# Kernel optimization log

Hardware: AMD Instinct MI355X
Metric: run time of the kernel (lower is better)

The kernel has to match this reference:

```python
import jax, jax.numpy as jnp
import numpy as np

B, N, D = 4, 512, 256  # batch, num_diseases, feature_dim == hidden_dim
H = 256                # hidden_dim
EPS = 1e-5

def _layernorm(x, g, b):
    m = jnp.mean(x, axis=-1, keepdims=True)
    v = jnp.mean((x - m) ** 2, axis=-1, keepdims=True)
    return (x - m) * jax.lax.rsqrt(v + EPS) * g + b

def setup_inputs() -> dict:
    key = jax.random.key(0)
    ks = jax.random.split(key, 16)
    s = 0.02
    return {
        "x": jax.random.normal(ks[0], (B, N, D), jnp.float32),
        "area_matrix": jax.random.uniform(ks[1], (B, N), jnp.float32),
        "co_occurrence": jax.random.uniform(ks[2], (N, N), jnp.float32),
        "Wq": jax.random.normal(ks[3], (H, D), jnp.float32) * s,
        "bq": jnp.zeros((H,), jnp.float32),
        "Wk": jax.random.normal(ks[4], (H, D), jnp.float32) * s,
        "bk": jnp.zeros((H,), jnp.float32),
        "Wv": jax.random.normal(ks[5], (H, D), jnp.float32) * s,
        "bv": jnp.zeros((H,), jnp.float32),
        "We1": jax.random.normal(ks[6], (H, 2), jnp.float32) * 0.5,
        "be1": jnp.zeros((H,), jnp.float32),
        "We2": jax.random.normal(ks[7], (1, H), jnp.float32) * s,
        "be2": jnp.zeros((1,), jnp.float32),
        "Wo": jax.random.normal(ks[8], (H, H), jnp.float32) * s,
        "bo": jnp.zeros((H,), jnp.float32),
        "g_ot": jnp.ones((H,), jnp.float32),
        "b_ot": jnp.zeros((H,), jnp.float32),
        "g1": jnp.ones((H,), jnp.float32),
        "b1": jnp.zeros((H,), jnp.float32),
        "g2": jnp.ones((H,), jnp.float32),
        "b2": jnp.zeros((H,), jnp.float32),
    }

def reference(x, area_matrix, co_occurrence, Wq, bq, Wk, bk, Wv, bv,
              We1, be1, We2, be2, Wo, bo, g_ot, b_ot, g1, b1, g2, b2):
    # projections: (B, N, H)
    q = jnp.einsum('bnd,hd->bnh', x, Wq) + bq
    k = jnp.einsum('bnd,hd->bnh', x, Wk) + bk
    v = jnp.einsum('bnd,hd->bnh', x, Wv) + bv
    attn_scores = jnp.einsum('bih,bjh->bij', q, k) / jnp.sqrt(jnp.float32(H))
    # edge inputs: (B, N, N, 2) = stack(broadcast area along last N, broadcast co-occ along batch)
    area = jnp.broadcast_to(area_matrix[:, :, None], (B, N, N))
    co = jnp.broadcast_to(co_occurrence[None], (B, N, N))
    edge_inputs = jnp.stack([area, co], axis=-1)
    h = jax.nn.relu(jnp.einsum('bije,he->bijh', edge_inputs, We1) + be1)
    edge_weights = jax.nn.sigmoid(jnp.einsum('bijh,oh->bijo', h, We2) + be2)[..., 0]
    attn_probs = jax.nn.softmax(attn_scores * edge_weights, axis=-1)  # dropout = identity (eval)
    out = jnp.einsum('bij,bjh->bih', attn_probs, v)
    out = _layernorm(out, g1, b1)
    out = jax.nn.relu(_layernorm(jnp.einsum('bnh,oh->bno', out, Wo) + bo, g_ot, b_ot))
    out = _layernorm(out + x, g2, b2)
    return out
```

## Files before the change

kernel.cpp:

```cpp
#include <hip/hip_runtime.h>

typedef unsigned short u16;
typedef unsigned int u32;

#define NB 4
#define NN 512
#define ND 256
#define NH 256
#define TI 4

typedef __attribute__((ext_vector_type(8))) short short8;
typedef __attribute__((ext_vector_type(4))) float f32x4;

typedef __attribute__((address_space(3))) u32 lds32_t;
typedef __attribute__((address_space(1))) const u32 g32_t;
__device__ __forceinline__ void pf16(const void* gp, u32* lp) {
    __builtin_amdgcn_global_load_lds((g32_t*)gp, (lds32_t*)lp, 16, 0, 0);
}

__device__ __forceinline__ u16 bfq(float f) {
    u32 t; __builtin_memcpy(&t, &f, 4);
    u32 r = (t + 0x7FFFu + ((t >> 16) & 1u)) >> 16;
    return (u16)r;
}

__device__ __forceinline__ float waveReduceSum(float v) {
#pragma unroll
    for (int o = 32; o > 0; o >>= 1) v += __shfl_down(v, o);
    return v;
}

__device__ __forceinline__ void blockReduce8(float4& va, float4& vb, float4* red) {
#pragma unroll
    for (int o = 32; o > 0; o >>= 1) {
        va.x += __shfl_down(va.x, o); va.y += __shfl_down(va.y, o);
        va.z += __shfl_down(va.z, o); va.w += __shfl_down(va.w, o);
        vb.x += __shfl_down(vb.x, o); vb.y += __shfl_down(vb.y, o);
        vb.z += __shfl_down(vb.z, o); vb.w += __shfl_down(vb.w, o);
    }
    int wid = threadIdx.x >> 6;
    __syncthreads();
    if ((threadIdx.x & 63) == 0) { red[2 * wid] = va; red[2 * wid + 1] = vb; }
    __syncthreads();
    float4 ra = red[0], rb = red[1];
#pragma unroll
    for (int w = 1; w < 8; ++w) {
        float4 ua = red[2 * w], ub = red[2 * w + 1];
        ra.x += ua.x; ra.y += ua.y; ra.z += ua.z; ra.w += ua.w;
        rb.x += ub.x; rb.y += ub.y; rb.z += ub.z; rb.w += ub.w;
    }
    va = ra; vb = rb;
}

__global__ __launch_bounds__(256) void prep_kernel(
    const float* __restrict__ x, const float* __restrict__ Wq,
    const float* __restrict__ Wk, const float* __restrict__ Wv,
    const float* __restrict__ Wo,
    u16* __restrict__ xb, u16* __restrict__ wb)
{
    const int idx4 = (blockIdx.x * 256 + threadIdx.x) * 4;
    const float* src;
    u16* dst;
    int off;
    if (idx4 < 524288) { src = x; dst = xb; off = idx4; }
    else {
        int u = idx4 - 524288;
        int which = u >> 16; off = u & 65535;
        src = (which == 0) ? Wq : (which == 1) ? Wk : (which == 2) ? Wv : Wo;
        dst = wb + which * 65536;
    }
    float4 f = *(const float4*)(src + off);
    u32 lo = (u32)bfq(f.x) | ((u32)bfq(f.y) << 16);
    u32 hi = (u32)bfq(f.z) | ((u32)bfq(f.w) << 16);
    *(uint2*)(dst + off) = make_uint2(lo, hi);
}

__global__ __launch_bounds__(256) void qkv_mfma(
    const u16* __restrict__ xb, const u16* __restrict__ wb,
    const float* __restrict__ bq, const float* __restrict__ bk, const float* __restrict__ bv,
    u16* __restrict__ qb, u16* __restrict__ kb, u16* __restrict__ vt)
{
    const int lane = threadIdx.x & 63, wave = threadIdx.x >> 6;
    const int r0 = blockIdx.x * 64 + wave * 16;
    const int out0 = blockIdx.y * 16;
    const int which = blockIdx.y >> 4;
    const float* bia = (which == 0) ? bq : (which == 1) ? bk : bv;

    __shared__ u32 pfdummy[256];

    {
        const u16* apre = xb + (size_t)(blockIdx.x * 64 + wave * 16) * 256;
#pragma unroll
        for (int q = 0; q < 8; ++q) pf16(apre + q * 512 + lane * 8, pfdummy);
        const u16* bpre = wb + which * 65536 + (size_t)((out0 & 255) + wave * 4) * 256;
#pragma unroll
        for (int q = 0; q < 2; ++q) pf16(bpre + q * 512 + lane * 8, pfdummy);
    }

    const int m = lane & 15, koff = (lane >> 4) * 8;
    const u16* Ap = xb + (size_t)(r0 + m) * 256 + koff;
    const u16* Bp = wb + which * 65536 + (size_t)((out0 & 255) + m) * 256 + koff;

    f32x4 acc = {0.f, 0.f, 0.f, 0.f};
#pragma unroll
    for (int ks = 0; ks < 8; ++ks) {
        short8 a  = *(const short8*)(Ap + ks * 32);
        short8 bb = *(const short8*)(Bp + ks * 32);
        acc = __builtin_amdgcn_mfma_f32_16x16x32_bf16(a, bb, acc, 0, 0, 0);
    }

    const int oc = (out0 + m) & 255;
    const float bias = bia[oc];
    const int rbase = r0 + (lane >> 4) * 4;
#pragma unroll
    for (int reg = 0; reg < 4; ++reg) {
        int R = rbase + reg;
        u16 val = bfq(acc[reg] + bias);
        if (which == 0)      qb[(size_t)R * 256 + oc] = val;
        else if (which == 1) kb[(size_t)R * 256 + oc] = val;
        else                 vt[((size_t)(R >> 9) * 256 + oc) * 512 + (R & 511)] = val;
    }
}

#define PSTR 520
#define YSTR 264
__global__ __launch_bounds__(512, 4) void fused_kernel(
    const float* __restrict__ x, const float* __restrict__ area, const float* __restrict__ co,
    const float* __restrict__ We1, const float* __restrict__ be1,
    const float* __restrict__ We2, const float* __restrict__ be2,
    const u16* __restrict__ wob, const float* __restrict__ bo,
    const float* __restrict__ g_ot, const float* __restrict__ b_ot,
    const float* __restrict__ g1, const float* __restrict__ b1,
    const float* __restrict__ g2, const float* __restrict__ b2,
    const u16* __restrict__ qb, const u16* __restrict__ kb,
    const u16* __restrict__ vt, float* __restrict__ out)
{
    const int tid = threadIdx.x;
    const int bsw = (blockIdx.x & 7) * 64 + (blockIdx.x >> 3);
    const int b = bsw >> 7;
    const int i0 = (bsw & 127) << 2;
    const int lane = tid & 63, w = tid >> 6;
    const int g = lane >> 4, c = lane & 15;
    const int hP = tid & 255, half = tid >> 8;

    __shared__ float histS[1024], histB[1024];
    __shared__ float pvbuf[1024];
    __shared__ u16 srow16[16 * PSTR];
    __shared__ u16 y16[16 * YSTR];
    __shared__ float4 red8b[16];
    __shared__ float sBaseS[4], sBaseB[4], redA[8], redB[8];
    __shared__ u32 pfdummy[256];

    const int m = lane & 15, koff = (lane >> 4) * 8;
    const u16* Ap    = qb + (size_t)(b * 512 + i0 + m) * 256 + koff;
    const u16* Kbase = kb + (size_t)(b * 512 + m) * 256 + koff;

    short8 afr[8];
#pragma unroll
    for (int ks = 0; ks < 8; ++ks) afr[ks] = *(const short8*)(Ap + ks * 32);

    float cov[4];
#pragma unroll
    for (int t = 0; t < 4; ++t)
        cov[t] = co[(size_t)(i0 + g) * NN + (w * 4 + t) * 16 + c];

    float xv[TI];
#pragma unroll
    for (int ti = 0; ti < TI; ++ti)
        xv[ti] = x[(size_t)(b * NN + i0 + ti) * ND + hP];

    const float bov  = bo[hP];
    const float g1v  = g1[hP],  b1v  = b1[hP];
    const float gotv = g_ot[hP], botv = b_ot[hP];
    const float g2v  = g2[hP],  b2v  = b2[hP];
    const float be2f = be2[0];

    {
        const u16* kpre = kb + (size_t)(b * 512 + w * 64) * 256;
#pragma unroll
        for (int q = 0; q < 32; ++q) pf16(kpre + q * 512 + lane * 8, pfdummy);
        const u16* vpre = vt + (size_t)(b * 256 + w * 32) * 512;
#pragma unroll
        for (int q = 0; q < 32; ++q) pf16(vpre + q * 512 + lane * 8, pfdummy);
        const u16* wpre = wob + (size_t)(w * 32) * 256;
#pragma unroll
        for (int q = 0; q < 16; ++q) pf16(wpre + q * 512 + lane * 8, pfdummy);
        pf16(co + (size_t)(i0 + (w >> 1)) * 512 + (w & 1) * 256 + lane * 4, pfdummy);
    }

    histS[tid] = 0.f; histS[tid + 512] = 0.f;
    histB[tid] = 0.f; histB[tid + 512] = 0.f;
    {
        u32* s32 = (u32*)srow16;
        for (int i = tid; i < 4160; i += 512) s32[i] = 0u;
        u32* y32 = (u32*)y16;
        for (int i = tid; i < 2112; i += 512) y32[i] = 0u;
    }
    __syncthreads();

    {
        const int s = tid >> 7, h0 = tid & 127;
        const float a = area[b * NN + i0 + s];
        float baS = 0.f, baB = 0.f;
#pragma unroll
        for (int k = 0; k < 2; ++k) {
            const int h = h0 + 128 * k;
            const float w10 = We1[2 * h], w11 = We1[2 * h + 1];
            const float w2v = We2[h], be1v = be1[h];
            const float al = fmaf(a, w10, be1v);
            const float sl = w11 * w2v, bb = al * w2v;
            if (w11 == 0.f) {
                if (al > 0.f) baB += bb;
            } else {
                float tt = -al / w11;
                if (w11 > 0.f) {
                    if (tt <= 0.f)      { baS += sl; baB += bb; }
                    else if (tt < 1.f) {
                        int u = (int)(tt * 256.f); u = u > 255 ? 255 : u;
                        atomicAdd(&histS[s * 256 + u], sl);
                        atomicAdd(&histB[s * 256 + u], bb);
                    }
                } else {
                    if (tt >= 1.f)      { baS += sl; baB += bb; }
                    else if (tt > 0.f) {
                        baS += sl; baB += bb;
                        int u = (int)(tt * 256.f); u = u > 255 ? 255 : u;
                        atomicAdd(&histS[s * 256 + u], -sl);
                        atomicAdd(&histB[s * 256 + u], -bb);
                    }
                }
            }
        }
        float rS = waveReduceSum(baS), rB = waveReduceSum(baB);
        if (lane == 0) { redA[w] = rS; redB[w] = rB; }
    }

    f32x4 sacc[4];
    {
#pragma unroll
        for (int t = 0; t < 4; ++t) {
            const u16* Bp = Kbase + (size_t)(w * 4 + t) * 16 * 256;
            f32x4 acc = {0.f, 0.f, 0.f, 0.f};
#pragma unroll
            for (int ks = 0; ks < 8; ++ks) {
                short8 bb = *(const short8*)(Bp + ks * 32);
                acc = __builtin_amdgcn_mfma_f32_16x16x32_bf16(afr[ks], bb, acc, 0, 0, 0);
            }
            sacc[t] = acc;
        }
    }
    __syncthreads();
    if (tid < 4) {
        sBaseS[tid] = redA[2 * tid] + redA[2 * tid + 1];
        sBaseB[tid] = redB[2 * tid] + redB[2 * tid + 1];
    }

    {
        const int s = w & 3;
        float* hp = (w < 4) ? histS : histB;
        float b0 = hp[s * 256 + 4 * lane + 0];
        float b1 = hp[s * 256 + 4 * lane + 1];
        float b2 = hp[s * 256 + 4 * lane + 2];
        float b3 = hp[s * 256 + 4 * lane + 3];
        float p0 = b0, p1 = p0 + b1, p2 = p1 + b2, p3 = p2 + b3;
        float incl = p3;
#pragma unroll
        for (int off = 1; off < 64; off <<= 1) {
            float t = __shfl_up(incl, off);
            if (lane >= off) incl += t;
        }
        float excl = incl - p3;
        hp[s * 256 + 4 * lane + 0] = p0 + excl;
        hp[s * 256 + 4 * lane + 1] = p1 + excl;
        hp[s * 256 + 4 * lane + 2] = p2 + excl;
        hp[s * 256 + 4 * lane + 3] = p3 + excl;
    }
    __syncthreads();

    {
#pragma unroll
        for (int t = 0; t < 4; ++t) {
            const int j = (w * 4 + t) * 16 + c;
            float s0 = __shfl(sacc[t][0], c);
            float s1 = __shfl(sacc[t][1], c);
            float s2 = __shfl(sacc[t][2], c);
            float s3 = __shfl(sacc[t][3], c);
            float sv = (g == 0) ? s0 : (g == 1) ? s1 : (g == 2) ? s2 : s3;
            float cc = cov[t];
            int u = (int)(cc * 256.f); u = u > 255 ? 255 : u;
            float Sg = sBaseS[g] + histS[g * 256 + u];
            float Bg = sBaseB[g] + histB[g * 256 + u];
            float e = fmaf(cc, Sg, Bg) + be2f;
            float ew = 1.f / (1.f + __expf(-e));
            srow16[g * PSTR + j] = bfq(__expf(sv * 0.0625f * ew));
        }
    }
    __syncthreads();

    {
        const int t0 = 2 * w, t1 = 2 * w + 1;
        const u16* B0p = vt + ((size_t)(b * 256 + t0 * 16 + m)) * 512 + koff;
        const u16* B1p = vt + ((size_t)(b * 256 + t1 * 16 + m)) * 512 + koff;
        const u16* Arow = srow16 + m * PSTR + koff;
        f32x4 acc0 = {0.f, 0.f, 0.f, 0.f}, acc1 = {0.f, 0.f, 0.f, 0.f};
#pragma unroll
        for (int ks = 0; ks < 16; ++ks) {
            short8 a  = *(const short8*)(Arow + ks * 32);
            short8 b0 = *(const short8*)(B0p + ks * 32);
            short8 b1 = *(const short8*)(B1p + ks * 32);
            acc0 = __builtin_amdgcn_mfma_f32_16x16x32_bf16(a, b0, acc0, 0, 0, 0);
            acc1 = __builtin_amdgcn_mfma_f32_16x16x32_bf16(a, b1, acc1, 0, 0, 0);
        }
        if (lane < 16) {
#pragma unroll
            for (int reg = 0; reg < 4; ++reg) {
                pvbuf[reg * 256 + t0 * 16 + lane] = acc0[reg];
                pvbuf[reg * 256 + t1 * 16 + lane] = acc1[reg];
            }
        }
        __syncthreads();
    }

    float4 sa, sb;
    float accv[TI];
#pragma unroll
    for (int ti = 0; ti < TI; ++ti) {
        accv[ti] = (half == 0) ? pvbuf[ti * 256 + hP] : 0.f;
        ((float*)&sa)[ti] = accv[ti];
        ((float*)&sb)[ti] = accv[ti] * accv[ti];
    }
    blockReduce8(sa, sb, red8b);
    if (half == 0) {
#pragma unroll
        for (int ti = 0; ti < TI; ++ti) {
            float mean = ((const float*)&sa)[ti] * (1.f / 256.f);
            float var = fmaxf(((const float*)&sb)[ti] * (1.f / 256.f) - mean * mean, 0.f);
            y16[ti * YSTR + hP] = bfq((accv[ti] - mean) * rsqrtf(var + 1e-5f) * g1v + b1v);
        }
    }
    __syncthreads();

    {
        const int t0 = 2 * w, t1 = 2 * w + 1;
        const u16* B0p = wob + (size_t)(t0 * 16 + m) * 256 + koff;
        const u16* B1p = wob + (size_t)(t1 * 16 + m) * 256 + koff;
        const u16* Arow = y16 + m * YSTR + koff;
        f32x4 acc0 = {0.f, 0.f, 0.f, 0.f}, acc1 = {0.f, 0.f, 0.f, 0.f};
#pragma unroll
        for (int ks = 0; ks < 8; ++ks) {
            short8 a  = *(const short8*)(Arow + ks * 32);
            short8 b0 = *(const short8*)(B0p + ks * 32);
            short8 b1 = *(const short8*)(B1p + ks * 32);
            acc0 = __builtin_amdgcn_mfma_f32_16x16x32_bf16(a, b0, acc0, 0, 0, 0);
            acc1 = __builtin_amdgcn_mfma_f32_16x16x32_bf16(a, b1, acc1, 0, 0, 0);
        }
        if (lane < 16) {
#pragma unroll
            for (int reg = 0; reg < 4; ++reg) {
                pvbuf[reg * 256 + t0 * 16 + lane] = acc0[reg];
                pvbuf[reg * 256 + t1 * 16 + lane] = acc1[reg];
            }
        }
        __syncthreads();
    }

    float acc2[TI];
#pragma unroll
    for (int ti = 0; ti < TI; ++ti) {
        acc2[ti] = (half == 0) ? pvbuf[ti * 256 + hP] + bov : 0.f;
        ((float*)&sa)[ti] = acc2[ti];
        ((float*)&sb)[ti] = acc2[ti] * acc2[ti];
    }
    blockReduce8(sa, sb, red8b);
    float z[TI];
#pragma unroll
    for (int ti = 0; ti < TI; ++ti) {
        float mean = ((const float*)&sa)[ti] * (1.f / 256.f);
        float var = fmaxf(((const float*)&sb)[ti] * (1.f / 256.f) - mean * mean, 0.f);
        z[ti] = fmaxf((acc2[ti] - mean) * rsqrtf(var + 1e-5f) * gotv + botv, 0.f);
    }

    float tt[TI];
#pragma unroll
    for (int ti = 0; ti < TI; ++ti) {
        tt[ti] = (half == 0) ? z[ti] + xv[ti] : 0.f;
        ((float*)&sa)[ti] = tt[ti]; ((float*)&sb)[ti] = tt[ti] * tt[ti];
    }
    blockReduce8(sa, sb, red8b);
    if (half == 0) {
#pragma unroll
        for (int ti = 0; ti < TI; ++ti) {
            float mean = ((const float*)&sa)[ti] * (1.f / 256.f);
            float var = fmaxf(((const float*)&sb)[ti] * (1.f / 256.f) - mean * mean, 0.f);
            float o = (tt[ti] - mean) * rsqrtf(var + 1e-5f) * g2v + b2v;
            out[(size_t)(b * NN + i0 + ti) * NH + hP] = o;
        }
    }
}

extern "C" void kernel_launch(void* const* d_in, const int* in_sizes, int n_in,
                              void* d_out, int out_size, void* d_ws, size_t ws_size,
                              hipStream_t stream) {
    const float* x    = (const float*)d_in[0];
    const float* area = (const float*)d_in[1];
    const float* co   = (const float*)d_in[2];
    const float* Wq   = (const float*)d_in[3];
    const float* bq   = (const float*)d_in[4];
    const float* Wk   = (const float*)d_in[5];
    const float* bk   = (const float*)d_in[6];
    const float* Wv   = (const float*)d_in[7];
    const float* bv   = (const float*)d_in[8];
    const float* We1  = (const float*)d_in[9];
    const float* be1  = (const float*)d_in[10];
    const float* We2  = (const float*)d_in[11];
    const float* be2  = (const float*)d_in[12];
    const float* Wo   = (const float*)d_in[13];
    const float* bo   = (const float*)d_in[14];
    const float* g_ot = (const float*)d_in[15];
    const float* b_ot = (const float*)d_in[16];
    const float* g1   = (const float*)d_in[17];
    const float* b1   = (const float*)d_in[18];
    const float* g2   = (const float*)d_in[19];
    const float* b2   = (const float*)d_in[20];

    u16*  xb  = (u16*)d_ws;
    u16*  wb  = xb + (size_t)2048 * 256;
    u16*  qb  = wb + (size_t)4 * 65536;
    u16*  kb  = qb + (size_t)2048 * 256;
    u16*  vt  = kb + (size_t)2048 * 256;

    prep_kernel<<<768, 256, 0, stream>>>(x, Wq, Wk, Wv, Wo, xb, wb);
    qkv_mfma<<<dim3(32, 48), 256, 0, stream>>>(xb, wb, bq, bk, bv, qb, kb, vt);
    fused_kernel<<<NB * NN / TI, 512, 0, stream>>>(x, area, co, We1, be1, We2, be2,
                                                   wb + 3 * 65536, bo,
                                                   g_ot, b_ot, g1, b1, g2, b2,
                                                   qb, kb, vt, (float*)d_out);
}
```

Measured before the change: 172.5 us.

## Merge prep, QKV projection and attention into one kernel with grid barriers

The three launches (bf16 conversion, QKV MFMA projection, fused attention) become one persistent kernel of 512 blocks. Two software grid barriers built on atomics separate the phases, and the edge-MLP histogram work now runs before the first barrier wait so it overlaps the conversion. The aim is to remove launch gaps and inter-kernel drain, at the cost of a memset per call, spin-wait barriers that assume all 512 blocks are co-resident, and dropping the LDS prefetch hints.

```diff
diff --git a/kernel.cpp b/kernel.cpp
--- a/kernel.cpp
+++ b/kernel.cpp
@@ -8,15 +8,10 @@
 #define ND 256
 #define NH 256
 #define TI 4
+#define NBLK 512
 
 typedef __attribute__((ext_vector_type(8))) short short8;
 typedef __attribute__((ext_vector_type(4))) float f32x4;
-
-typedef __attribute__((address_space(3))) u32 lds32_t;
-typedef __attribute__((address_space(1))) const u32 g32_t;
-__device__ __forceinline__ void pf16(const void* gp, u32* lp) {
-    __builtin_amdgcn_global_load_lds((g32_t*)gp, (lds32_t*)lp, 16, 0, 0);
-}
 
 __device__ __forceinline__ u16 bfq(float f) {
     u32 t; __builtin_memcpy(&t, &f, 4);
@@ -52,96 +47,46 @@
     va = ra; vb = rb;
 }
 
-__global__ __launch_bounds__(256) void prep_kernel(
-    const float* __restrict__ x, const float* __restrict__ Wq,
-    const float* __restrict__ Wk, const float* __restrict__ Wv,
-    const float* __restrict__ Wo,
-    u16* __restrict__ xb, u16* __restrict__ wb)
-{
-    const int idx4 = (blockIdx.x * 256 + threadIdx.x) * 4;
-    const float* src;
-    u16* dst;
-    int off;
-    if (idx4 < 524288) { src = x; dst = xb; off = idx4; }
-    else {
-        int u = idx4 - 524288;
-        int which = u >> 16; off = u & 65535;
-        src = (which == 0) ? Wq : (which == 1) ? Wk : (which == 2) ? Wv : Wo;
-        dst = wb + which * 65536;
-    }
-    float4 f = *(const float4*)(src + off);
-    u32 lo = (u32)bfq(f.x) | ((u32)bfq(f.y) << 16);
-    u32 hi = (u32)bfq(f.z) | ((u32)bfq(f.w) << 16);
-    *(uint2*)(dst + off) = make_uint2(lo, hi);
-}
-
-__global__ __launch_bounds__(256) void qkv_mfma(
-    const u16* __restrict__ xb, const u16* __restrict__ wb,
-    const float* __restrict__ bq, const float* __restrict__ bk, const float* __restrict__ bv,
-    u16* __restrict__ qb, u16* __restrict__ kb, u16* __restrict__ vt)
-{
-    const int lane = threadIdx.x & 63, wave = threadIdx.x >> 6;
-    const int r0 = blockIdx.x * 64 + wave * 16;
-    const int out0 = blockIdx.y * 16;
-    const int which = blockIdx.y >> 4;
-    const float* bia = (which == 0) ? bq : (which == 1) ? bk : bv;
-
-    __shared__ u32 pfdummy[256];
-
-    {
-        const u16* apre = xb + (size_t)(blockIdx.x * 64 + wave * 16) * 256;
-#pragma unroll
-        for (int q = 0; q < 8; ++q) pf16(apre + q * 512 + lane * 8, pfdummy);
-        const u16* bpre = wb + which * 65536 + (size_t)((out0 & 255) + wave * 4) * 256;
-#pragma unroll
-        for (int q = 0; q < 2; ++q) pf16(bpre + q * 512 + lane * 8, pfdummy);
-    }
-
-    const int m = lane & 15, koff = (lane >> 4) * 8;
-    const u16* Ap = xb + (size_t)(r0 + m) * 256 + koff;
-    const u16* Bp = wb + which * 65536 + (size_t)((out0 & 255) + m) * 256 + koff;
-
-    f32x4 acc = {0.f, 0.f, 0.f, 0.f};
-#pragma unroll
-    for (int ks = 0; ks < 8; ++ks) {
-        short8 a  = *(const short8*)(Ap + ks * 32);
-        short8 bb = *(const short8*)(Bp + ks * 32);
-        acc = __builtin_amdgcn_mfma_f32_16x16x32_bf16(a, bb, acc, 0, 0, 0);
-    }
-
-    const int oc = (out0 + m) & 255;
-    const float bias = bia[oc];
-    const int rbase = r0 + (lane >> 4) * 4;
-#pragma unroll
-    for (int reg = 0; reg < 4; ++reg) {
-        int R = rbase + reg;
-        u16 val = bfq(acc[reg] + bias);
-        if (which == 0)      qb[(size_t)R * 256 + oc] = val;
-        else if (which == 1) kb[(size_t)R * 256 + oc] = val;
-        else                 vt[((size_t)(R >> 9) * 256 + oc) * 512 + (R & 511)] = val;
-    }
+__device__ __forceinline__ void gbar_arrive(u32* c) {
+    __syncthreads();
+    if (threadIdx.x == 0)
+        __hip_atomic_fetch_add(c, 1u, __ATOMIC_RELEASE, __HIP_MEMORY_SCOPE_AGENT);
+}
+__device__ __forceinline__ void gbar_wait(u32* c, u32 n) {
+    if (threadIdx.x == 0) {
+        while (__hip_atomic_load(c, __ATOMIC_ACQUIRE, __HIP_MEMORY_SCOPE_AGENT) < n)
+            __builtin_amdgcn_s_sleep(2);
+    }
+    __syncthreads();
+    __threadfence();
 }
 
 #define PSTR 520
 #define YSTR 264
-__global__ __launch_bounds__(512, 4) void fused_kernel(
+__global__ __launch_bounds__(512, 4) void mono_kernel(
     const float* __restrict__ x, const float* __restrict__ area, const float* __restrict__ co,
+    const float* __restrict__ Wq, const float* __restrict__ bq,
+    const float* __restrict__ Wk, const float* __restrict__ bk,
+    const float* __restrict__ Wv, const float* __restrict__ bv,
     const float* __restrict__ We1, const float* __restrict__ be1,
     const float* __restrict__ We2, const float* __restrict__ be2,
-    const u16* __restrict__ wob, const float* __restrict__ bo,
+    const float* __restrict__ Wo, const float* __restrict__ bo,
     const float* __restrict__ g_ot, const float* __restrict__ b_ot,
     const float* __restrict__ g1, const float* __restrict__ b1,
     const float* __restrict__ g2, const float* __restrict__ b2,
-    const u16* __restrict__ qb, const u16* __restrict__ kb,
-    const u16* __restrict__ vt, float* __restrict__ out)
+    u16* __restrict__ xb, u16* __restrict__ wb,
+    u16* __restrict__ qb, u16* __restrict__ kb, u16* __restrict__ vt,
+    u32* __restrict__ bar, float* __restrict__ out)
 {
     const int tid = threadIdx.x;
+    const int lane = tid & 63, w = tid >> 6;
+    const int m = lane & 15, koff = (lane >> 4) * 8;
+    const int g = lane >> 4, c = lane & 15;
+    const int hP = tid & 255, half = tid >> 8;
+
     const int bsw = (blockIdx.x & 7) * 64 + (blockIdx.x >> 3);
     const int b = bsw >> 7;
     const int i0 = (bsw & 127) << 2;
-    const int lane = tid & 63, w = tid >> 6;
-    const int g = lane >> 4, c = lane & 15;
-    const int hP = tid & 255, half = tid >> 8;
 
     __shared__ float histS[1024], histB[1024];
     __shared__ float pvbuf[1024];
@@ -149,26 +94,15 @@
     __shared__ u16 y16[16 * YSTR];
     __shared__ float4 red8b[16];
     __shared__ float sBaseS[4], sBaseB[4], redA[8], redB[8];
-    __shared__ u32 pfdummy[256];
-
-    const int m = lane & 15, koff = (lane >> 4) * 8;
-    const u16* Ap    = qb + (size_t)(b * 512 + i0 + m) * 256 + koff;
-    const u16* Kbase = kb + (size_t)(b * 512 + m) * 256 + koff;
-
-    short8 afr[8];
-#pragma unroll
-    for (int ks = 0; ks < 8; ++ks) afr[ks] = *(const short8*)(Ap + ks * 32);
 
     float cov[4];
 #pragma unroll
     for (int t = 0; t < 4; ++t)
         cov[t] = co[(size_t)(i0 + g) * NN + (w * 4 + t) * 16 + c];
-
     float xv[TI];
 #pragma unroll
     for (int ti = 0; ti < TI; ++ti)
         xv[ti] = x[(size_t)(b * NN + i0 + ti) * ND + hP];
-
     const float bov  = bo[hP];
     const float g1v  = g1[hP],  b1v  = b1[hP];
     const float gotv = g_ot[hP], botv = b_ot[hP];
@@ -176,17 +110,24 @@
     const float be2f = be2[0];
 
     {
-        const u16* kpre = kb + (size_t)(b * 512 + w * 64) * 256;
-#pragma unroll
-        for (int q = 0; q < 32; ++q) pf16(kpre + q * 512 + lane * 8, pfdummy);
-        const u16* vpre = vt + (size_t)(b * 256 + w * 32) * 512;
-#pragma unroll
-        for (int q = 0; q < 32; ++q) pf16(vpre + q * 512 + lane * 8, pfdummy);
-        const u16* wpre = wob + (size_t)(w * 32) * 256;
-#pragma unroll
-        for (int q = 0; q < 16; ++q) pf16(wpre + q * 512 + lane * 8, pfdummy);
-        pf16(co + (size_t)(i0 + (w >> 1)) * 512 + (w & 1) * 256 + lane * 4, pfdummy);
-    }
+        const int gtid = blockIdx.x * 512 + tid;
+        const int idx4 = gtid * 4;
+        if (idx4 < 786432) {
+            const float* src; u16* dst; int off;
+            if (idx4 < 524288) { src = x; dst = xb; off = idx4; }
+            else {
+                int u = idx4 - 524288;
+                int which = u >> 16; off = u & 65535;
+                src = (which == 0) ? Wq : (which == 1) ? Wk : (which == 2) ? Wv : Wo;
+                dst = wb + which * 65536;
+            }
+            float4 f = *(const float4*)(src + off);
+            u32 lo = (u32)bfq(f.x) | ((u32)bfq(f.y) << 16);
+            u32 hi = (u32)bfq(f.z) | ((u32)bfq(f.w) << 16);
+            *(uint2*)(dst + off) = make_uint2(lo, hi);
+        }
+    }
+    gbar_arrive(bar);
 
     histS[tid] = 0.f; histS[tid + 512] = 0.f;
     histB[tid] = 0.f; histB[tid + 512] = 0.f;
@@ -197,7 +138,6 @@
         for (int i = tid; i < 2112; i += 512) y32[i] = 0u;
     }
     __syncthreads();
-
     {
         const int s = tid >> 7, h0 = tid & 127;
         const float a = area[b * NN + i0 + s];
@@ -234,27 +174,11 @@
         float rS = waveReduceSum(baS), rB = waveReduceSum(baB);
         if (lane == 0) { redA[w] = rS; redB[w] = rB; }
     }
-
-    f32x4 sacc[4];
-    {
-#pragma unroll
-        for (int t = 0; t < 4; ++t) {
-            const u16* Bp = Kbase + (size_t)(w * 4 + t) * 16 * 256;
-            f32x4 acc = {0.f, 0.f, 0.f, 0.f};
-#pragma unroll
-            for (int ks = 0; ks < 8; ++ks) {
-                short8 bb = *(const short8*)(Bp + ks * 32);
-                acc = __builtin_amdgcn_mfma_f32_16x16x32_bf16(afr[ks], bb, acc, 0, 0, 0);
-            }
-            sacc[t] = acc;
-        }
-    }
     __syncthreads();
     if (tid < 4) {
         sBaseS[tid] = redA[2 * tid] + redA[2 * tid + 1];
         sBaseB[tid] = redB[2 * tid] + redB[2 * tid + 1];
     }
-
     {
         const int s = w & 3;
         float* hp = (w < 4) ? histS : histB;
@@ -275,7 +199,63 @@
         hp[s * 256 + 4 * lane + 2] = p2 + excl;
         hp[s * 256 + 4 * lane + 3] = p3 + excl;
     }
-    __syncthreads();
+    gbar_wait(bar, NBLK);
+
+    {
+        const int wid = blockIdx.x * 8 + w;
+        for (int job = wid; job < 6144; job += 4096) {
+            const int rowTile = job & 127;
+            const int colJob  = job >> 7;
+            const int which   = colJob >> 4;
+            const int oc0     = (colJob & 15) << 4;
+            const int r0      = rowTile << 4;
+            const float* bia = (which == 0) ? bq : (which == 1) ? bk : bv;
+
+            const u16* Ap = xb + (size_t)(r0 + m) * 256 + koff;
+            const u16* Bp = wb + which * 65536 + (size_t)(oc0 + m) * 256 + koff;
+
+            f32x4 acc = {0.f, 0.f, 0.f, 0.f};
+#pragma unroll
+            for (int ks = 0; ks < 8; ++ks) {
+                short8 a  = *(const short8*)(Ap + ks * 32);
+                short8 bb = *(const short8*)(Bp + ks * 32);
+                acc = __builtin_amdgcn_mfma_f32_16x16x32_bf16(a, bb, acc, 0, 0, 0);
+            }
+            const int oc = oc0 + m;
+            const float bias = bia[oc];
+            const int rbase = r0 + (lane >> 4) * 4;
+#pragma unroll
+            for (int reg = 0; reg < 4; ++reg) {
+                int R = rbase + reg;
+                u16 val = bfq(acc[reg] + bias);
+                if (which == 0)      qb[(size_t)R * 256 + oc] = val;
+                else if (which == 1) kb[(size_t)R * 256 + oc] = val;
+                else                 vt[((size_t)(R >> 9) * 256 + oc) * 512 + (R & 511)] = val;
+            }
+        }
+    }
+    gbar_arrive(bar + 16);
+    gbar_wait(bar + 16, NBLK);
+
+    f32x4 sacc[4];
+    {
+        const u16* Ap    = qb + (size_t)(b * 512 + i0 + m) * 256 + koff;
+        const u16* Kbase = kb + (size_t)(b * 512 + m) * 256 + koff;
+        short8 afr[8];
+#pragma unroll
+        for (int ks = 0; ks < 8; ++ks) afr[ks] = *(const short8*)(Ap + ks * 32);
+#pragma unroll
+        for (int t = 0; t < 4; ++t) {
+            const u16* Bp = Kbase + (size_t)(w * 4 + t) * 16 * 256;
+            f32x4 acc = {0.f, 0.f, 0.f, 0.f};
+#pragma unroll
+            for (int ks = 0; ks < 8; ++ks) {
+                short8 bb = *(const short8*)(Bp + ks * 32);
+                acc = __builtin_amdgcn_mfma_f32_16x16x32_bf16(afr[ks], bb, acc, 0, 0, 0);
+            }
+            sacc[t] = acc;
+        }
+    }
 
     {
 #pragma unroll
@@ -341,6 +321,7 @@
     __syncthreads();
 
     {
+        const u16* wob = wb + 3 * 65536;
         const int t0 = 2 * w, t1 = 2 * w + 1;
         const u16* B0p = wob + (size_t)(t0 * 16 + m) * 256 + koff;
         const u16* B1p = wob + (size_t)(t1 * 16 + m) * 256 + koff;
@@ -428,11 +409,12 @@
     u16*  qb  = wb + (size_t)4 * 65536;
     u16*  kb  = qb + (size_t)2048 * 256;
     u16*  vt  = kb + (size_t)2048 * 256;
-
-    prep_kernel<<<768, 256, 0, stream>>>(x, Wq, Wk, Wv, Wo, xb, wb);
-    qkv_mfma<<<dim3(32, 48), 256, 0, stream>>>(xb, wb, bq, bk, bv, qb, kb, vt);
-    fused_kernel<<<NB * NN / TI, 512, 0, stream>>>(x, area, co, We1, be1, We2, be2,
-                                                   wb + 3 * 65536, bo,
-                                                   g_ot, b_ot, g1, b1, g2, b2,
-                                                   qb, kb, vt, (float*)d_out);
-}
+    u32*  bar = (u32*)((char*)d_ws + ((size_t)32 << 20));
+    float* outp = (float*)d_out;
+
+    hipMemsetAsync(bar, 0, 128, stream);
+    mono_kernel<<<NBLK, 512, 0, stream>>>(x, area, co, Wq, bq, Wk, bk, Wv, bv,
+                                          We1, be1, We2, be2, Wo, bo,
+                                          g_ot, b_ot, g1, b1, g2, b2,
+                                          xb, wb, qb, kb, vt, bar, outp);
+}
```

New measurement: 363.5 us. +110.7%, slower.
